# Kernel tuning notes

Measured on AMD Instinct MI355X. Metric: run time of the kernel, lower is better.

The kernel has to match this reference:

```python
import jax, jax.numpy as jnp
import numpy as np

B, C_IN, H, W = 32, 64, 64, 64
D, O, S_SP, K = 256, 512, 4, 3


def setup_inputs() -> dict:
    key = jax.random.key(0)
    k1, k2, k3, k4, k5 = jax.random.split(key, 5)
    x = jax.random.normal(k1, (B, C_IN, H, W), dtype=jnp.float32)
    dictionary = jax.random.normal(k2, (D, C_IN, K, K), dtype=jnp.float32)
    lookup_coefficients = jax.random.normal(k3, (O, S_SP), dtype=jnp.float32)
    bias = jax.random.normal(k4, (O,), dtype=jnp.float32)
    lookup_indices = jax.random.randint(k5, (O, S_SP), 0, D)
    return {
        "x": x,
        "dictionary": dictionary,
        "lookup_coefficients": lookup_coefficients,
        "bias": bias,
        "lookup_indices": lookup_indices,
    }


def reference(x, dictionary, lookup_coefficients, bias, lookup_indices):
    # Dictionary conv: S has shape [B, D, H, W] (stride 1, padding 1, 3x3 kernel)
    S = jax.lax.conv_general_dilated(
        x, dictionary,
        window_strides=(1, 1),
        padding=((1, 1), (1, 1)),
        dimension_numbers=("NCHW", "OIHW", "NCHW"),
    )
    # Build dense [O, D] combine matrix via scatter-add (duplicate indices
    # accumulate, matching the original += loop), then one GEMM.
    rows = jnp.arange(O)[:, None]  # [O, 1] broadcast against [O, sparsity]
    Wc = jnp.zeros((O, D), dtype=S.dtype).at[rows, lookup_indices].add(lookup_coefficients)
    out = jnp.einsum("bdhw,od->bohw", S, Wc)
    return out + bias[None, :, None, None]
```

## Files before the change

### kernel.cpp

```cpp
#include <hip/hip_runtime.h>
#include <stdint.h>

#define NB 32
#define NC 64
#define NH 64
#define NW 64
#define NO 512
#define HP 66

typedef __bf16 bf16x8 __attribute__((ext_vector_type(8)));
typedef short  s16x8  __attribute__((ext_vector_type(8)));
typedef float  f32x4  __attribute__((ext_vector_type(4)));

__device__ __forceinline__ uint16_t f2bf(float f) {
  uint32_t u = __builtin_bit_cast(uint32_t, f);
  u += 0x7fffu + ((u >> 16) & 1u);
  return (uint16_t)(u >> 16);
}

__device__ __forceinline__ void gld16(const uint16_t* g, uint16_t* l) {
  __builtin_amdgcn_global_load_lds(
      (const __attribute__((address_space(1))) void*)(g),
      (__attribute__((address_space(3))) void*)(l), 16, 0, 0);
}

__global__ void k_prep(const float* __restrict__ dict,
                       const float* __restrict__ coef,
                       const int*   __restrict__ idx,
                       const float* __restrict__ x,
                       uint16_t*    __restrict__ Wl,
                       uint16_t*    __restrict__ xh) {
  const int bid = blockIdx.x;
  const int t = threadIdx.x;
  if (bid < NO) {
    __shared__ float tmp[576];
    const int o = bid;
#pragma unroll
    for (int j = 0; j < 3; ++j) {
      const int id = t + j * 256;
      if (id < 576) {
        float v = 0.f;
#pragma unroll
        for (int s = 0; s < 4; ++s)
          v += coef[o * 4 + s] * dict[idx[o * 4 + s] * 576 + id];
        tmp[id] = v;
      }
    }
    __syncthreads();
#pragma unroll
    for (int j = 0; j < 3; ++j) {
      const int id = t + j * 256;
      if (id < 576) {
        const int c = id & 63, p = id >> 6;
        const int sl = ((p * NO + o) * 8 + ((c >> 3) ^ (o & 7))) * 8 + (c & 7);
        Wl[sl] = f2bf(tmp[c * 9 + p]);
      }
    }
    return;
  }
  const int bh = bid - NO;
  const int b = bh / HP, hp = bh % HP;
  uint16_t* row = xh + (size_t)(b * HP + hp) * 4096;
  int4* r4 = reinterpret_cast<int4*>(row);
  if (hp == 0 || hp == HP - 1) {
    r4[t]       = int4{0, 0, 0, 0};
    r4[t + 256] = int4{0, 0, 0, 0};
    return;
  }
  __shared__ float tile[64][65];
  const int h = hp - 1;
  const int w = t & 63;
#pragma unroll
  for (int c = (t >> 6); c < 64; c += 4)
    tile[c][w] = x[((size_t)(b * NC + c) * NH + h) * NW + w];
  __syncthreads();
#pragma unroll
  for (int i = 0; i < 2; ++i) {
    const int s = t + i * 256;
    const int w2 = s >> 3, cb = s & 7;
    uint32_t d[4];
#pragma unroll
    for (int j = 0; j < 4; ++j) {
      const uint32_t lo = f2bf(tile[cb * 8 + 2 * j][w2]);
      const uint32_t hi = f2bf(tile[cb * 8 + 2 * j + 1][w2]);
      d[j] = lo | (hi << 16);
    }
    r4[w2 * 8 + (cb ^ (w2 & 7))] =
        int4{(int)d[0], (int)d[1], (int)d[2], (int)d[3]};
  }
}

__global__ __launch_bounds__(512, 2) void k_conv(
    const uint16_t* __restrict__ xh,
    const uint16_t* __restrict__ Wl,
    const float*    __restrict__ bias,
    float*          __restrict__ out) {
  __shared__ __align__(16) uint16_t xs[10 * 66 * 64];
  __shared__ __align__(16) uint16_t as[3 * 128 * 64];

  const int t = threadIdx.x;
  const int lane = t & 63;
  const int wid  = t >> 6;
  const int blk = blockIdx.x;
  const int gy = (blk & 7) * 32 + (blk >> 3);
  const int b  = gy >> 3;
  const int h0 = (gy & 7) * 8;

  if (t < 160) {
    const int r = t >> 4, sl = (t >> 3) & 1, j = t & 7;
    reinterpret_cast<int4*>(xs)[r * 528 + sl * 520 + j] = int4{0, 0, 0, 0};
  }
  {
    const uint16_t* srow = xh + (size_t)(b * HP + h0 + wid) * 4096;
    uint16_t* drow = xs + wid * 4224 + 64;
#pragma unroll
    for (int k = 0; k < 8; ++k)
      gld16(srow + k * 512 + lane * 8, drow + k * 512);
    const int r2 = 8 + (wid >> 2);
    const int kb = (wid & 3) * 2;
    const uint16_t* srow2 = xh + (size_t)(b * HP + h0 + r2) * 4096;
    uint16_t* drow2 = xs + r2 * 4224 + 64;
    gld16(srow2 + kb * 512 + lane * 8, drow2 + kb * 512);
    gld16(srow2 + (kb + 1) * 512 + lane * 8, drow2 + (kb + 1) * 512);
  }
  auto stage_a = [&](int orr, int g) {
    const int O0 = orr * 128;
#pragma unroll
    for (int j = 0; j < 6; ++j) {
      const int c = wid * 6 + j;
      const int tap = c >> 4, k = c & 15;
      const uint16_t* src =
          Wl + (size_t)(tap * 3 + g) * 32768 + (O0 + k * 8) * 64;
      gld16(src + lane * 8, as + tap * 8192 + k * 512);
    }
  };
  stage_a(0, 0);

  const int wm  = wid & 1;
  const int wn  = wid >> 1;
  const int l15 = lane & 15;
  const int lg  = lane >> 4;

  float bvv[4][4];
#pragma unroll
  for (int orr = 0; orr < 4; ++orr)
#pragma unroll
    for (int ob = 0; ob < 4; ++ob)
      bvv[orr][ob] = bias[orr * 128 + wm * 64 + ob * 16 + l15];

  f32x4 acc[8][4];

  __syncthreads();

#pragma unroll
  for (int orr = 0; orr < 4; ++orr) {
    const int O0 = orr * 128;
#pragma unroll
    for (int pb = 0; pb < 8; ++pb)
#pragma unroll
      for (int ob = 0; ob < 4; ++ob)
        acc[pb][ob] = (f32x4){0.f, 0.f, 0.f, 0.f};

#pragma unroll
    for (int g = 0; g < 3; ++g) {
      const int dw = g - 1;
#pragma unroll
      for (int q = 0; q < 2; ++q) {
        const int cbB = (q * 4 + lg) ^ ((l15 + dw) & 7);
        const uint16_t* xb = xs + (l15 + dw + 1) * 64 + cbB * 8;
        bf16x8 braw[4][4];
#pragma unroll
        for (int rr = 0; rr < 4; ++rr)
#pragma unroll
          for (int nw = 0; nw < 4; ++nw)
            braw[rr][nw] = __builtin_bit_cast(bf16x8,
                *reinterpret_cast<const s16x8*>(
                    xb + (wn * 2 + rr) * 4224 + nw * 1024));
        const int cbA = (q * 4 + lg) ^ (l15 & 7);
        const uint16_t* ab = as + (wm * 64 + l15) * 64 + cbA * 8;
#pragma unroll
        for (int dh = 0; dh < 3; ++dh) {
          bf16x8 af[4];
#pragma unroll
          for (int ob = 0; ob < 4; ++ob)
            af[ob] = __builtin_bit_cast(bf16x8,
                *reinterpret_cast<const s16x8*>(
                    ab + dh * 8192 + ob * 1024));
#pragma unroll
          for (int pb = 0; pb < 8; ++pb)
#pragma unroll
            for (int ob = 0; ob < 4; ++ob)
              acc[pb][ob] = __builtin_amdgcn_mfma_f32_16x16x32_bf16(
                  braw[(pb >> 2) + dh][pb & 3], af[ob], acc[pb][ob], 0, 0, 0);
        }
      }
      if (g < 2) {
        asm volatile("s_waitcnt lgkmcnt(0)" ::: "memory");
        __builtin_amdgcn_s_barrier();
        stage_a(orr, g + 1);
        __syncthreads();
      }
    }

    asm volatile("s_waitcnt lgkmcnt(0)" ::: "memory");
    __builtin_amdgcn_s_barrier();
    if (orr < 3) stage_a(orr + 1, 0);
    asm volatile("" ::: "memory");
    {
      const int hb = h0 + wn * 2;
#pragma unroll
      for (int pb = 0; pb < 8; ++pb) {
#pragma unroll
        for (int ob = 0; ob < 4; ++ob) {
          const int o = O0 + wm * 64 + ob * 16 + l15;
          f32x4 v = acc[pb][ob];
          const float bv = bvv[orr][ob];
          v[0] += bv; v[1] += bv; v[2] += bv; v[3] += bv;
          float* dst = out +
              ((size_t)(b * NO + o) * NH + hb + (pb >> 2)) * NW +
              (pb & 3) * 16 + lg * 4;
          __builtin_nontemporal_store(v, reinterpret_cast<f32x4*>(dst));
        }
      }
    }
    asm volatile("" ::: "memory");
    if (orr < 3) {
      asm volatile("s_waitcnt vmcnt(32)" ::: "memory");
      __builtin_amdgcn_s_barrier();
    }
  }
}

extern "C" void kernel_launch(void* const* d_in, const int* in_sizes, int n_in,
                              void* d_out, int out_size, void* d_ws, size_t ws_size,
                              hipStream_t stream) {
  const float* x    = (const float*)d_in[0];
  const float* dict = (const float*)d_in[1];
  const float* coef = (const float*)d_in[2];
  const float* bias = (const float*)d_in[3];
  const int*   idx  = (const int*)d_in[4];
  float* out = (float*)d_out;

  uint16_t* xh = (uint16_t*)d_ws;
  uint16_t* Wl = (uint16_t*)((char*)d_ws + (18u << 20));

  hipLaunchKernelGGL(k_prep, dim3(NO + NB * HP), dim3(256), 0, stream,
                     dict, coef, idx, x, Wl, xh);
  hipLaunchKernelGGL(k_conv, dim3(256), dim3(512), 0, stream,
                     xh, Wl, bias, out);
}
```

Measured before the change: 123.4 us.

## Convolve with the dictionary, then apply the sparse combine from LDS

Instead of folding the sparse coefficients into 512 dense 3x3 filters, the conv now runs against the 256 dictionary atoms, roughly halving the MFMA work. The intermediate S tile is stored to shared memory in bf16 with a swizzle. Each output channel then gathers its 4 indexed rows, scales them by the coefficients and adds the bias. This trades compute for an extra LDS gather phase, bf16 rounding of S, and a larger shared-memory footprint that limits the kernel to one block per CU.

```diff
diff --git a/kernel.cpp b/kernel.cpp
--- a/kernel.cpp
+++ b/kernel.cpp
@@ -6,17 +6,28 @@
 #define NH 64
 #define NW 64
 #define NO 512
+#define ND 256
 #define HP 66
 
 typedef __bf16 bf16x8 __attribute__((ext_vector_type(8)));
 typedef short  s16x8  __attribute__((ext_vector_type(8)));
 typedef float  f32x4  __attribute__((ext_vector_type(4)));
+typedef uint32_t u32x2 __attribute__((ext_vector_type(2)));
 
 __device__ __forceinline__ uint16_t f2bf(float f) {
   uint32_t u = __builtin_bit_cast(uint32_t, f);
   u += 0x7fffu + ((u >> 16) & 1u);
   return (uint16_t)(u >> 16);
 }
+__device__ __forceinline__ uint32_t pk2(float a, float b) {
+  return (uint32_t)f2bf(a) | ((uint32_t)f2bf(b) << 16);
+}
+__device__ __forceinline__ float ubf_lo(uint32_t u) {
+  return __builtin_bit_cast(float, u << 16);
+}
+__device__ __forceinline__ float ubf_hi(uint32_t u) {
+  return __builtin_bit_cast(float, u & 0xffff0000u);
+}
 
 __device__ __forceinline__ void gld16(const uint16_t* g, uint16_t* l) {
   __builtin_amdgcn_global_load_lds(
@@ -25,40 +36,25 @@
 }
 
 __global__ void k_prep(const float* __restrict__ dict,
-                       const float* __restrict__ coef,
-                       const int*   __restrict__ idx,
                        const float* __restrict__ x,
-                       uint16_t*    __restrict__ Wl,
+                       uint16_t*    __restrict__ Wd,
                        uint16_t*    __restrict__ xh) {
   const int bid = blockIdx.x;
   const int t = threadIdx.x;
-  if (bid < NO) {
-    __shared__ float tmp[576];
-    const int o = bid;
-#pragma unroll
-    for (int j = 0; j < 3; ++j) {
-      const int id = t + j * 256;
-      if (id < 576) {
-        float v = 0.f;
-#pragma unroll
-        for (int s = 0; s < 4; ++s)
-          v += coef[o * 4 + s] * dict[idx[o * 4 + s] * 576 + id];
-        tmp[id] = v;
-      }
-    }
-    __syncthreads();
+  if (bid < ND) {
+    const int d = bid;
 #pragma unroll
     for (int j = 0; j < 3; ++j) {
       const int id = t + j * 256;
       if (id < 576) {
         const int c = id & 63, p = id >> 6;
-        const int sl = ((p * NO + o) * 8 + ((c >> 3) ^ (o & 7))) * 8 + (c & 7);
-        Wl[sl] = f2bf(tmp[c * 9 + p]);
+        const int sl = ((p * ND + d) * 8 + ((c >> 3) ^ (d & 7))) * 8 + (c & 7);
+        Wd[sl] = f2bf(dict[d * 576 + c * 9 + p]);
       }
     }
     return;
   }
-  const int bh = bid - NO;
+  const int bh = bid - ND;
   const int b = bh / HP, hp = bh % HP;
   uint16_t* row = xh + (size_t)(b * HP + hp) * 4096;
   int4* r4 = reinterpret_cast<int4*>(row);
@@ -78,156 +74,154 @@
   for (int i = 0; i < 2; ++i) {
     const int s = t + i * 256;
     const int w2 = s >> 3, cb = s & 7;
-    uint32_t d[4];
-#pragma unroll
-    for (int j = 0; j < 4; ++j) {
-      const uint32_t lo = f2bf(tile[cb * 8 + 2 * j][w2]);
-      const uint32_t hi = f2bf(tile[cb * 8 + 2 * j + 1][w2]);
-      d[j] = lo | (hi << 16);
-    }
+    uint32_t dd[4];
+#pragma unroll
+    for (int j = 0; j < 4; ++j)
+      dd[j] = pk2(tile[cb * 8 + 2 * j][w2], tile[cb * 8 + 2 * j + 1][w2]);
     r4[w2 * 8 + (cb ^ (w2 & 7))] =
-        int4{(int)d[0], (int)d[1], (int)d[2], (int)d[3]};
+        int4{(int)dd[0], (int)dd[1], (int)dd[2], (int)dd[3]};
   }
 }
 
 __global__ __launch_bounds__(512, 2) void k_conv(
     const uint16_t* __restrict__ xh,
-    const uint16_t* __restrict__ Wl,
+    const uint16_t* __restrict__ Wd,
+    const float*    __restrict__ coef,
+    const int*      __restrict__ idx,
     const float*    __restrict__ bias,
     float*          __restrict__ out) {
-  __shared__ __align__(16) uint16_t xs[10 * 66 * 64];
-  __shared__ __align__(16) uint16_t as[3 * 128 * 64];
+  __shared__ __align__(16) uint16_t smem[74496];
+  uint16_t* xs  = smem;
+  uint16_t* asw = smem + 25344;
+  uint8_t*  Sb  = (uint8_t*)smem;
 
   const int t = threadIdx.x;
   const int lane = t & 63;
   const int wid  = t >> 6;
-  const int blk = blockIdx.x;
-  const int gy = (blk & 7) * 32 + (blk >> 3);
-  const int b  = gy >> 3;
-  const int h0 = (gy & 7) * 8;
-
-  if (t < 160) {
+  const int flat = blockIdx.x;
+  const int s    = (flat & 7) * 64 + (flat >> 3);
+  const int b    = s >> 4;
+  const int hq   = s & 15;
+  const int h0p  = hq * 4;
+
+  if (t < 96) {
     const int r = t >> 4, sl = (t >> 3) & 1, j = t & 7;
     reinterpret_cast<int4*>(xs)[r * 528 + sl * 520 + j] = int4{0, 0, 0, 0};
   }
   {
-    const uint16_t* srow = xh + (size_t)(b * HP + h0 + wid) * 4096;
-    uint16_t* drow = xs + wid * 4224 + 64;
-#pragma unroll
-    for (int k = 0; k < 8; ++k)
-      gld16(srow + k * 512 + lane * 8, drow + k * 512);
-    const int r2 = 8 + (wid >> 2);
-    const int kb = (wid & 3) * 2;
-    const uint16_t* srow2 = xh + (size_t)(b * HP + h0 + r2) * 4096;
-    uint16_t* drow2 = xs + r2 * 4224 + 64;
-    gld16(srow2 + kb * 512 + lane * 8, drow2 + kb * 512);
-    gld16(srow2 + (kb + 1) * 512 + lane * 8, drow2 + (kb + 1) * 512);
-  }
-  auto stage_a = [&](int orr, int g) {
-    const int O0 = orr * 128;
 #pragma unroll
     for (int j = 0; j < 6; ++j) {
-      const int c = wid * 6 + j;
-      const int tap = c >> 4, k = c & 15;
-      const uint16_t* src =
-          Wl + (size_t)(tap * 3 + g) * 32768 + (O0 + k * 8) * 64;
-      gld16(src + lane * 8, as + tap * 8192 + k * 512);
+      const int ch = wid * 6 + j;
+      const int r = ch >> 3, k = ch & 7;
+      gld16(xh + (size_t)(b * HP + h0p + r) * 4096 + k * 512 + lane * 8,
+            xs + r * 4224 + 64 + k * 512);
+    }
+  }
+  auto stage_a = [&](int g) {
+#pragma unroll
+    for (int j = 0; j < 12; ++j) {
+      const int ch = wid * 12 + j;
+      const int tap = ch >> 5, k = ch & 31;
+      gld16(Wd + (size_t)(tap * 3 + g) * 16384 + k * 512 + lane * 8,
+            asw + tap * 16384 + k * 512);
     }
   };
-  stage_a(0, 0);
-
-  const int wm  = wid & 1;
-  const int wn  = wid >> 1;
+  stage_a(0);
+
+  const int wd  = wid & 3;
+  const int wn  = wid >> 2;
   const int l15 = lane & 15;
   const int lg  = lane >> 4;
 
-  float bvv[4][4];
-#pragma unroll
-  for (int orr = 0; orr < 4; ++orr)
-#pragma unroll
-    for (int ob = 0; ob < 4; ++ob)
-      bvv[orr][ob] = bias[orr * 128 + wm * 64 + ob * 16 + l15];
-
   f32x4 acc[8][4];
-
-  __syncthreads();
-
-#pragma unroll
-  for (int orr = 0; orr < 4; ++orr) {
-    const int O0 = orr * 128;
-#pragma unroll
-    for (int pb = 0; pb < 8; ++pb)
-#pragma unroll
-      for (int ob = 0; ob < 4; ++ob)
-        acc[pb][ob] = (f32x4){0.f, 0.f, 0.f, 0.f};
-
-#pragma unroll
-    for (int g = 0; g < 3; ++g) {
-      const int dw = g - 1;
-#pragma unroll
-      for (int q = 0; q < 2; ++q) {
-        const int cbB = (q * 4 + lg) ^ ((l15 + dw) & 7);
-        const uint16_t* xb = xs + (l15 + dw + 1) * 64 + cbB * 8;
-        bf16x8 braw[4][4];
-#pragma unroll
-        for (int rr = 0; rr < 4; ++rr)
-#pragma unroll
-          for (int nw = 0; nw < 4; ++nw)
-            braw[rr][nw] = __builtin_bit_cast(bf16x8,
-                *reinterpret_cast<const s16x8*>(
-                    xb + (wn * 2 + rr) * 4224 + nw * 1024));
-        const int cbA = (q * 4 + lg) ^ (l15 & 7);
-        const uint16_t* ab = as + (wm * 64 + l15) * 64 + cbA * 8;
-#pragma unroll
-        for (int dh = 0; dh < 3; ++dh) {
-          bf16x8 af[4];
-#pragma unroll
-          for (int ob = 0; ob < 4; ++ob)
-            af[ob] = __builtin_bit_cast(bf16x8,
-                *reinterpret_cast<const s16x8*>(
-                    ab + dh * 8192 + ob * 1024));
-#pragma unroll
-          for (int pb = 0; pb < 8; ++pb)
-#pragma unroll
-            for (int ob = 0; ob < 4; ++ob)
-              acc[pb][ob] = __builtin_amdgcn_mfma_f32_16x16x32_bf16(
-                  braw[(pb >> 2) + dh][pb & 3], af[ob], acc[pb][ob], 0, 0, 0);
-        }
+#pragma unroll
+  for (int pb = 0; pb < 8; ++pb)
+#pragma unroll
+    for (int db = 0; db < 4; ++db)
+      acc[pb][db] = (f32x4){0.f, 0.f, 0.f, 0.f};
+
+  __syncthreads();
+
+#pragma unroll
+  for (int g = 0; g < 3; ++g) {
+    const int dw = g - 1;
+#pragma unroll
+    for (int q = 0; q < 2; ++q) {
+      const int cbB = (q * 4 + lg) ^ ((l15 + dw) & 7);
+      const uint16_t* xb = xs + (l15 + dw + 1) * 64 + cbB * 8;
+      bf16x8 braw[4][4];
+#pragma unroll
+      for (int rr = 0; rr < 4; ++rr)
+#pragma unroll
+        for (int nw = 0; nw < 4; ++nw)
+          braw[rr][nw] = __builtin_bit_cast(bf16x8,
+              *reinterpret_cast<const s16x8*>(
+                  xb + (wn * 2 + rr) * 4224 + nw * 1024));
+      const int cbA = (q * 4 + lg) ^ (l15 & 7);
+      const uint16_t* ab = asw + (wd * 64 + l15) * 64 + cbA * 8;
+#pragma unroll
+      for (int dh = 0; dh < 3; ++dh) {
+        bf16x8 af[4];
+#pragma unroll
+        for (int db = 0; db < 4; ++db)
+          af[db] = __builtin_bit_cast(bf16x8,
+              *reinterpret_cast<const s16x8*>(
+                  ab + dh * 16384 + db * 1024));
+#pragma unroll
+        for (int pb = 0; pb < 8; ++pb)
+#pragma unroll
+          for (int db = 0; db < 4; ++db)
+            acc[pb][db] = __builtin_amdgcn_mfma_f32_16x16x32_bf16(
+                braw[(pb >> 2) + dh][pb & 3], af[db], acc[pb][db], 0, 0, 0);
       }
-      if (g < 2) {
-        asm volatile("s_waitcnt lgkmcnt(0)" ::: "memory");
-        __builtin_amdgcn_s_barrier();
-        stage_a(orr, g + 1);
-        __syncthreads();
-      }
-    }
-
-    asm volatile("s_waitcnt lgkmcnt(0)" ::: "memory");
-    __builtin_amdgcn_s_barrier();
-    if (orr < 3) stage_a(orr + 1, 0);
-    asm volatile("" ::: "memory");
-    {
-      const int hb = h0 + wn * 2;
-#pragma unroll
-      for (int pb = 0; pb < 8; ++pb) {
-#pragma unroll
-        for (int ob = 0; ob < 4; ++ob) {
-          const int o = O0 + wm * 64 + ob * 16 + l15;
-          f32x4 v = acc[pb][ob];
-          const float bv = bvv[orr][ob];
-          v[0] += bv; v[1] += bv; v[2] += bv; v[3] += bv;
-          float* dst = out +
-              ((size_t)(b * NO + o) * NH + hb + (pb >> 2)) * NW +
-              (pb & 3) * 16 + lg * 4;
-          __builtin_nontemporal_store(v, reinterpret_cast<f32x4*>(dst));
-        }
-      }
-    }
-    asm volatile("" ::: "memory");
-    if (orr < 3) {
-      asm volatile("s_waitcnt vmcnt(32)" ::: "memory");
-      __builtin_amdgcn_s_barrier();
-    }
+    }
+    if (g < 2) {
+      __syncthreads();
+      stage_a(g + 1);
+      __syncthreads();
+    }
+  }
+
+  __syncthreads();
+#pragma unroll
+  for (int pb = 0; pb < 8; ++pb) {
+#pragma unroll
+    for (int db = 0; db < 4; ++db) {
+      const int d   = wd * 64 + db * 16 + l15;
+      const int pix = (wn * 2 + (pb >> 2)) * 64 + (pb & 3) * 16 + lg * 4;
+      u32x2 u;
+      u[0] = pk2(acc[pb][db][0], acc[pb][db][1]);
+      u[1] = pk2(acc[pb][db][2], acc[pb][db][3]);
+      *reinterpret_cast<u32x2*>(
+          Sb + d * 512 + ((pix * 2) ^ ((d & 7) << 4))) = u;
+    }
+  }
+  __syncthreads();
+
+  const int hrow = lane >> 4;
+  const int wcol = (lane & 15) * 4;
+#pragma unroll 4
+  for (int oo = 0; oo < 64; ++oo) {
+    const int o = wid * 64 + oo;
+    const int4 iv = *reinterpret_cast<const int4*>(idx + o * 4);
+    const f32x4 cv = *reinterpret_cast<const f32x4*>(coef + o * 4);
+    const float bv = bias[o];
+    f32x4 v = {bv, bv, bv, bv};
+#define GATH(ROW, CS) do {                                                  \
+      const int r_ = (ROW);                                                 \
+      const u32x2 u_ = *reinterpret_cast<const u32x2*>(                     \
+          Sb + r_ * 512 + ((lane * 8) ^ ((r_ & 7) << 4)));                  \
+      const float c_ = (CS);                                                \
+      v[0] += c_ * ubf_lo(u_[0]);  v[1] += c_ * ubf_hi(u_[0]);              \
+      v[2] += c_ * ubf_lo(u_[1]);  v[3] += c_ * ubf_hi(u_[1]);              \
+    } while (0)
+    GATH(iv.x, cv[0]);
+    GATH(iv.y, cv[1]);
+    GATH(iv.z, cv[2]);
+    GATH(iv.w, cv[3]);
+#undef GATH
+    float* dst = out + ((size_t)(b * NO + o) * NH + hq * 4 + hrow) * NW + wcol;
+    __builtin_nontemporal_store(v, reinterpret_cast<f32x4*>(dst));
   }
 }
 
@@ -242,10 +236,10 @@
   float* out = (float*)d_out;
 
   uint16_t* xh = (uint16_t*)d_ws;
-  uint16_t* Wl = (uint16_t*)((char*)d_ws + (18u << 20));
-
-  hipLaunchKernelGGL(k_prep, dim3(NO + NB * HP), dim3(256), 0, stream,
-                     dict, coef, idx, x, Wl, xh);
-  hipLaunchKernelGGL(k_conv, dim3(256), dim3(512), 0, stream,
-                     xh, Wl, bias, out);
-}
+  uint16_t* Wd = (uint16_t*)((char*)d_ws + (18u << 20));
+
+  hipLaunchKernelGGL(k_prep, dim3(ND + NB * HP), dim3(256), 0, stream,
+                     dict, x, Wd, xh);
+  hipLaunchKernelGGL(k_conv, dim3(512), dim3(512), 0, stream,
+                     xh, Wd, coef, idx, bias, out);
+}
```

Result: faster. 99.67 us (-19.2%).
